# Optimization experiments

Measured on AMD Instinct MI355X. Metric: run time of the kernel, lower is better.

The kernel has to match this reference:

```python
import jax, jax.numpy as jnp
import numpy as np

E = 1024   # embed_dim
H = 16     # num_heads
D = E // H # head_dim = 64
S = 8192   # cache length
LN_EPS = 1e-6  # flax LayerNorm default


def _ln(x, scale, bias):
    m = jnp.mean(x, axis=-1, keepdims=True)
    v = jnp.mean(jnp.square(x - m), axis=-1, keepdims=True)
    return (x - m) * jax.lax.rsqrt(v + LN_EPS) * scale + bias


def setup_inputs() -> dict:
    key = jax.random.key(0)
    ks = jax.random.split(key, 16)
    w = lambda k, shape: jax.random.normal(k, shape, jnp.float32) * 0.02
    return {
        "x": jax.random.normal(ks[0], (E,), jnp.float32),
        "cache": jax.random.normal(ks[1], (2, S, H, D), jnp.float32),
        "Wv": w(ks[2], (E, E)), "bv": jnp.zeros((E,), jnp.float32),
        "Wq": w(ks[3], (E, E)), "bq": jnp.zeros((E,), jnp.float32),
        "Wk": w(ks[4], (E, E)), "bk": jnp.zeros((E,), jnp.float32),
        "Wo": w(ks[5], (E, E)), "bo": jnp.zeros((E,), jnp.float32),
        "W1": w(ks[6], (E, E)), "b1": jnp.zeros((E,), jnp.float32),
        "W2": w(ks[7], (E, E)), "b2": jnp.zeros((E,), jnp.float32),
        "ln1_s": jnp.ones((E,), jnp.float32), "ln1_b": jnp.zeros((E,), jnp.float32),
        "ln2_s": jnp.ones((E,), jnp.float32), "ln2_b": jnp.zeros((E,), jnp.float32),
        "eval_flag": 1,
    }


def reference(x, cache, Wv, bv, Wq, bq, Wk, bk, Wo, bo,
              W1, b1, W2, b2, ln1_s, ln1_b, ln2_s, ln2_b, eval_flag):
    # --- attention with shifting KV cache ---
    v_i = (x @ Wv + bv).reshape(1, H, D)
    q_i = (x @ Wq + bq).reshape(H, D)
    k_i = (x @ Wk + bk).reshape(1, H, D)
    v = jnp.concatenate((cache[0, 1:], v_i), axis=0)  # [S, H, D]
    k = jnp.concatenate((cache[1, 1:], k_i), axis=0)  # [S, H, D]
    mask = jnp.any(v != 0, axis=(1, 2))               # [S]
    attn = jnp.einsum('hd,khd->hk', q_i, k) / jnp.sqrt(jnp.float32(D))
    attn = jnp.where(mask, attn, -jnp.inf)
    attn = jax.nn.softmax(attn, axis=-1)              # [H, S]
    values = jnp.einsum('hk,khd->hd', attn, v).reshape(E)
    out_i = values @ Wo + bo
    new_cache = jnp.stack([v, k])                     # [2, S, H, D]

    # --- residual + LN + FFN (dropout deterministic => identity) ---
    h = _ln(x + out_i, ln1_s, ln1_b)
    ff = jax.nn.relu(h @ W1 + b1) @ W2 + b2
    h = _ln(h + ff, ln2_s, ln2_b)
    return (h, new_cache)
```

## Files before the change

### kernel.cpp

```cpp
#include <hip/hip_runtime.h>
#include <hip/hip_bf16.h>

#define SLEN 8192
#define EDIM 1024
#define NB   1024

typedef float f4 __attribute__((ext_vector_type(4)));


__device__ inline float2 blockSum256_2(float2 v, float2* lds) {
#pragma unroll
    for (int off = 32; off; off >>= 1) {
        v.x += __shfl_xor(v.x, off);
        v.y += __shfl_xor(v.y, off);
    }
    int w = threadIdx.x >> 6, ln = threadIdx.x & 63;
    __syncthreads();
    if (ln == 0) lds[w] = v;
    __syncthreads();
    float2 s;
    s.x = lds[0].x + lds[1].x + lds[2].x + lds[3].x;
    s.y = lds[0].y + lds[1].y + lds[2].y + lds[3].y;
    return s;
}

__device__ inline float2 blockSum1024_2(float2 v, float2* lds) {
#pragma unroll
    for (int off = 32; off; off >>= 1) {
        v.x += __shfl_xor(v.x, off);
        v.y += __shfl_xor(v.y, off);
    }
    int w = threadIdx.x >> 6, ln = threadIdx.x & 63;
    __syncthreads();
    if (ln == 0) lds[w] = v;
    __syncthreads();
    float2 s = {0.f, 0.f};
#pragma unroll
    for (int i = 0; i < 16; ++i) { s.x += lds[i].x; s.y += lds[i].y; }
    return s;
}

__global__ __launch_bounds__(256) void qkv_partial(
    const float* __restrict__ Wq, const float* __restrict__ Wk,
    const float* __restrict__ Wv, const float* __restrict__ x,
    float* __restrict__ part) {
    int cg = blockIdx.x;
    int m = cg >> 2;
    const float* W = (m == 0) ? Wq : ((m == 1) ? Wk : Wv);
    int col = (cg & 3) * 256 + threadIdx.x;
    int r0 = blockIdx.y * 64;
    float acc = 0.f;
#pragma unroll 8
    for (int r = 0; r < 64; ++r)
        acc = fmaf(x[r0 + r], W[(r0 + r) * EDIM + col], acc);
    part[((size_t)m * 16 + blockIdx.y) * EDIM + col] = acc;
}

__global__ __launch_bounds__(1024) void qkv_combine(
    const float* __restrict__ part,
    const float* __restrict__ bq, const float* __restrict__ bk,
    const float* __restrict__ bv,
    float* __restrict__ qs, float* __restrict__ ki, float* __restrict__ vi) {
    int m = blockIdx.x, t = threadIdx.x;
    float v = 0.f;
#pragma unroll
    for (int sl = 0; sl < 16; ++sl) v += part[((size_t)m * 16 + sl) * EDIM + t];
    if (m == 0) qs[t] = (v + bq[t]) * 0.125f;
    else if (m == 1) ki[t] = v + bk[t];
    else vi[t] = v + bv[t];
}

__global__ __launch_bounds__(512) void attn_main(
    const float* __restrict__ cache,
    const float* __restrict__ qs,
    const float* __restrict__ ki, const float* __restrict__ vi,
    float* __restrict__ nv, float* __restrict__ nk,
    float* __restrict__ m2, float* __restrict__ l2, float* __restrict__ acc2) {
    __shared__ float sm[8][16];
    __shared__ float mlM[16], mlL[16];
    __shared__ float sacc[8][16][64];
    int tid = threadIdx.x;
    int w = tid >> 6, ld = tid & 63;
    int s = blockIdx.x * 8 + w;

    bool last = (s >= SLEN - 1);
    const float* vsrc = last ? vi : cache + (size_t)(s + 1) * EDIM;
    const float* ksrc = last ? ki : cache + (size_t)(SLEN + s + 1) * EDIM;

    f4 vv[4], kv[4], q4[4];
#pragma unroll
    for (int it = 0; it < 4; ++it)
        vv[it] = __builtin_nontemporal_load((const f4*)(vsrc + it * 256 + ld * 4));
#pragma unroll
    for (int it = 0; it < 4; ++it)
        kv[it] = __builtin_nontemporal_load((const f4*)(ksrc + it * 256 + ld * 4));
#pragma unroll
    for (int it = 0; it < 4; ++it)
        q4[it] = *(const f4*)(qs + it * 256 + ld * 4);

    unsigned nzb = 0u;
#pragma unroll
    for (int it = 0; it < 4; ++it) {
        __builtin_nontemporal_store(vv[it], (f4*)(nv + (size_t)s * EDIM + it * 256 + ld * 4));
        nzb |= __float_as_uint(vv[it].x) | __float_as_uint(vv[it].y) |
               __float_as_uint(vv[it].z) | __float_as_uint(vv[it].w);
    }
    float sc[4];
#pragma unroll
    for (int it = 0; it < 4; ++it) {
        __builtin_nontemporal_store(kv[it], (f4*)(nk + (size_t)s * EDIM + it * 256 + ld * 4));
        float d = q4[it].x * kv[it].x + q4[it].y * kv[it].y +
                  q4[it].z * kv[it].z + q4[it].w * kv[it].w;
        d += __shfl_xor(d, 1);
        d += __shfl_xor(d, 2);
        d += __shfl_xor(d, 4);
        d += __shfl_xor(d, 8);
        sc[it] = d;
    }
    if (__ballot(nzb != 0u) == 0ull) {
#pragma unroll
        for (int it = 0; it < 4; ++it) sc[it] = -1e30f;
    }
    if ((ld & 15) == 0) {
#pragma unroll
        for (int it = 0; it < 4; ++it) sm[w][it * 4 + (ld >> 4)] = sc[it];
    }
    __syncthreads();

    if (tid < 16) {
        float M = sm[0][tid];
#pragma unroll
        for (int ww = 1; ww < 8; ++ww) M = fmaxf(M, sm[ww][tid]);
        float L = 0.f;
#pragma unroll
        for (int ww = 0; ww < 8; ++ww) L += __expf(sm[ww][tid] - M);
        mlM[tid] = M; mlL[tid] = L;
    }
    __syncthreads();

#pragma unroll
    for (int it = 0; it < 4; ++it) {
        int h = it * 4 + (ld >> 4);
        float wg = __expf(sc[it] - mlM[h]);
        *(f4*)&sacc[w][h][(ld & 15) * 4] =
            (f4){wg * vv[it].x, wg * vv[it].y, wg * vv[it].z, wg * vv[it].w};
    }
    __syncthreads();

#pragma unroll
    for (int j = 0; j < 2; ++j) {
        int h = 2 * w + j;
        float a = 0.f;
#pragma unroll
        for (int ww = 0; ww < 8; ++ww) a += sacc[ww][h][ld];
        acc2[((size_t)blockIdx.x * 16 + h) * 64 + ld] = a;
        if (ld == 0) {
            m2[blockIdx.x * 16 + h] = mlM[h];
            l2[blockIdx.x * 16 + h] = mlL[h];
        }
    }
}

__global__ __launch_bounds__(256) void attn_red(
    const float* __restrict__ m2, const float* __restrict__ l2,
    const float* __restrict__ acc2,
    float* __restrict__ m3, float* __restrict__ l3, float* __restrict__ acc3) {
    __shared__ float sM[4], sL[4], sA[4][64];
    int h = blockIdx.x, g = blockIdx.y;
    int t = threadIdx.x, w = t >> 6, ld = t & 63;
    int p0 = g * 64 + w * 16;

    float mv[16];
#pragma unroll
    for (int i = 0; i < 16; ++i) mv[i] = m2[(p0 + i) * 16 + h];
    float lm = -1e30f;
#pragma unroll
    for (int i = 0; i < 16; ++i) lm = fmaxf(lm, mv[i]);
    float ll = 0.f, la = 0.f;
#pragma unroll
    for (int i = 0; i < 16; ++i) {
        float e = __expf(mv[i] - lm);
        ll += e * l2[(p0 + i) * 16 + h];
        la += e * acc2[(size_t)(p0 + i) * 1024 + (size_t)h * 64 + ld];
    }
    if (ld == 0) { sM[w] = lm; sL[w] = ll; }
    sA[w][ld] = la;
    __syncthreads();
    if (w == 0) {
        float M = fmaxf(fmaxf(sM[0], sM[1]), fmaxf(sM[2], sM[3]));
        float L = 0.f, a = 0.f;
#pragma unroll
        for (int w4 = 0; w4 < 4; ++w4) {
            float e = __expf(sM[w4] - M);
            L += e * sL[w4];
            a += e * sA[w4][ld];
        }
        acc3[((size_t)g * 16 + h) * 64 + ld] = a;
        if (ld == 0) { m3[g * 16 + h] = M; l3[g * 16 + h] = L; }
    }
}

__global__ __launch_bounds__(256) void gemv_wo(
    const float* __restrict__ Wo,
    const float* __restrict__ m3, const float* __restrict__ l3,
    const float* __restrict__ acc3, float* __restrict__ part) {
    __shared__ float vals[64];
    int by = blockIdx.y;
    int t = threadIdx.x;
    float M = -1e30f;
#pragma unroll
    for (int g = 0; g < 16; ++g) M = fmaxf(M, m3[g * 16 + by]);
    float L = 0.f;
#pragma unroll
    for (int g = 0; g < 16; ++g) L += __expf(m3[g * 16 + by] - M) * l3[g * 16 + by];
    if (t < 64) {
        float a = 0.f;
#pragma unroll
        for (int g = 0; g < 16; ++g)
            a += __expf(m3[g * 16 + by] - M) * acc3[((size_t)g * 16 + by) * 64 + t];
        vals[t] = a / L;
    }
    __syncthreads();
    int col = blockIdx.x * 256 + t;
    float acc = 0.f;
#pragma unroll 8
    for (int r = 0; r < 64; ++r)
        acc = fmaf(vals[r], Wo[(size_t)(by * 64 + r) * EDIM + col], acc);
    part[(size_t)by * EDIM + col] = acc;
}

__global__ __launch_bounds__(256) void gemv_w1(
    const float* __restrict__ W1, const float* __restrict__ gp1,
    const float* __restrict__ bo, const float* __restrict__ x,
    const float* __restrict__ ln1s, const float* __restrict__ ln1b,
    float* __restrict__ h1, float* __restrict__ part) {
    __shared__ float r_l[1024];
    __shared__ float2 red[4];
    __shared__ float vals[64];
    int t = threadIdx.x;
    float2 ss = {0.f, 0.f};
#pragma unroll
    for (int j = 0; j < 4; ++j) {
        int i = t + 256 * j;
        float v = x[i] + bo[i];
#pragma unroll
        for (int sl = 0; sl < 16; ++sl) v += gp1[(size_t)sl * EDIM + i];
        r_l[i] = v;
        ss.x += v; ss.y += v * v;
    }
    float2 s = blockSum256_2(ss, red);
    float mean = s.x * (1.f / 1024.f);
    float var = s.y * (1.f / 1024.f) - mean * mean;
    float rstd = rsqrtf(var + 1e-6f);
    int by = blockIdx.y;
    if (t < 64) {
        int row = by * 64 + t;
        float hv = (r_l[row] - mean) * rstd * ln1s[row] + ln1b[row];
        vals[t] = hv;
        if (blockIdx.x == 0) h1[row] = hv;
    }
    __syncthreads();
    int col = blockIdx.x * 256 + t;
    float acc = 0.f;
#pragma unroll 8
    for (int r = 0; r < 64; ++r)
        acc = fmaf(vals[r], W1[(size_t)(by * 64 + r) * EDIM + col], acc);
    part[(size_t)by * EDIM + col] = acc;
}

__global__ __launch_bounds__(256) void gemv_w2(
    const float* __restrict__ W2, const float* __restrict__ gp2,
    const float* __restrict__ b1, float* __restrict__ part) {
    __shared__ float vals[64];
    int by = blockIdx.y;
    int t = threadIdx.x;
    if (t < 64) {
        int r = by * 64 + t;
        float v = b1[r];
#pragma unroll
        for (int sl = 0; sl < 16; ++sl) v += gp2[(size_t)sl * EDIM + r];
        vals[t] = fmaxf(v, 0.f);
    }
    __syncthreads();
    int col = blockIdx.x * 256 + t;
    float acc = 0.f;
#pragma unroll 8
    for (int r = 0; r < 64; ++r)
        acc = fmaf(vals[r], W2[(size_t)(by * 64 + r) * EDIM + col], acc);
    part[(size_t)by * EDIM + col] = acc;
}

__global__ __launch_bounds__(1024) void combine_ln(
    const float* __restrict__ part, const float* __restrict__ bias,
    const float* __restrict__ resid, const float* __restrict__ g,
    const float* __restrict__ b, float* __restrict__ out) {
    __shared__ float2 lds[16];
    int t = threadIdx.x;
    float v = bias[t];
#pragma unroll
    for (int sl = 0; sl < 16; ++sl) v += part[(size_t)sl * EDIM + t];
    float r = resid[t] + v;
    float2 s = blockSum1024_2((float2){r, r * r}, lds);
    float mean = s.x * (1.f / 1024.f);
    float var = s.y * (1.f / 1024.f) - mean * mean;
    out[t] = (r - mean) * rsqrtf(var + 1e-6f) * g[t] + b[t];
}

extern "C" void kernel_launch(void* const* d_in, const int* in_sizes, int n_in,
                              void* d_out, int out_size, void* d_ws, size_t ws_size,
                              hipStream_t stream) {
    const float* x     = (const float*)d_in[0];
    const float* cache = (const float*)d_in[1];
    const float* Wv    = (const float*)d_in[2];
    const float* bv    = (const float*)d_in[3];
    const float* Wq    = (const float*)d_in[4];
    const float* bq    = (const float*)d_in[5];
    const float* Wk    = (const float*)d_in[6];
    const float* bk    = (const float*)d_in[7];
    const float* Wo    = (const float*)d_in[8];
    const float* bo    = (const float*)d_in[9];
    const float* W1    = (const float*)d_in[10];
    const float* b1    = (const float*)d_in[11];
    const float* W2    = (const float*)d_in[12];
    const float* b2    = (const float*)d_in[13];
    const float* ln1s  = (const float*)d_in[14];
    const float* ln1b  = (const float*)d_in[15];
    const float* ln2s  = (const float*)d_in[16];
    const float* ln2b  = (const float*)d_in[17];

    float* out = (float*)d_out;
    float* nv = out + 1024;
    float* nk = out + 1024 + (size_t)SLEN * EDIM;

    float* w      = (float*)d_ws;
    float* qs     = w;
    float* ki     = qs + 1024;
    float* vi     = ki + 1024;
    float* qkvp   = vi + 1024;
    float* m2     = qkvp + 48 * 1024;
    float* l2     = m2 + (size_t)NB * 16;
    float* acc2   = l2 + (size_t)NB * 16;
    float* m3     = acc2 + (size_t)NB * 1024;
    float* l3     = m3 + 256;
    float* acc3   = l3 + 256;
    float* h1     = acc3 + 16 * 1024;
    float* gp1    = h1 + 1024;
    float* gp2    = gp1 + 16 * 1024;
    float* gp3    = gp2 + 16 * 1024;

    qkv_partial<<<dim3(12, 16), 256, 0, stream>>>(Wq, Wk, Wv, x, qkvp);
    qkv_combine<<<3, 1024, 0, stream>>>(qkvp, bq, bk, bv, qs, ki, vi);
    attn_main<<<NB, 512, 0, stream>>>(cache, qs, ki, vi, nv, nk, m2, l2, acc2);
    attn_red<<<dim3(16, 16), 256, 0, stream>>>(m2, l2, acc2, m3, l3, acc3);
    gemv_wo<<<dim3(4, 16), 256, 0, stream>>>(Wo, m3, l3, acc3, gp1);
    gemv_w1<<<dim3(4, 16), 256, 0, stream>>>(W1, gp1, bo, x, ln1s, ln1b, h1, gp2);
    gemv_w2<<<dim3(4, 16), 256, 0, stream>>>(W2, gp2, b1, gp3);
    combine_ln<<<1, 1024, 0, stream>>>(gp3, b2, h1, ln2s, ln2b, out);
}
```

Before: 61.13 us.

## Fold QKV combine into attention and fuse tail kernels into one cooperative launch

The qkv_combine kernel is removed: every attention block now sums the Q partials itself into shared memory, and the last block also builds the new k/v row. The attention reduction, Wo, W1 and W2 GEMVs and the final LayerNorm are merged into one cooperative kernel of 256 blocks separated by grid.sync, cutting eight launches down to three. The aim is to remove launch gaps and inter-kernel drain costs. The cost is redundant Q-partial reads in every attention block and grid-wide barrier overhead.

```diff
diff --git a/kernel.cpp b/kernel.cpp
--- a/kernel.cpp
+++ b/kernel.cpp
@@ -1,5 +1,8 @@
 #include <hip/hip_runtime.h>
+#include <hip/hip_cooperative_groups.h>
 #include <hip/hip_bf16.h>
+
+namespace cg = cooperative_groups;
 
 #define SLEN 8192
 #define EDIM 1024
@@ -24,30 +27,14 @@
     return s;
 }
 
-__device__ inline float2 blockSum1024_2(float2 v, float2* lds) {
-#pragma unroll
-    for (int off = 32; off; off >>= 1) {
-        v.x += __shfl_xor(v.x, off);
-        v.y += __shfl_xor(v.y, off);
-    }
-    int w = threadIdx.x >> 6, ln = threadIdx.x & 63;
-    __syncthreads();
-    if (ln == 0) lds[w] = v;
-    __syncthreads();
-    float2 s = {0.f, 0.f};
-#pragma unroll
-    for (int i = 0; i < 16; ++i) { s.x += lds[i].x; s.y += lds[i].y; }
-    return s;
-}
-
 __global__ __launch_bounds__(256) void qkv_partial(
     const float* __restrict__ Wq, const float* __restrict__ Wk,
     const float* __restrict__ Wv, const float* __restrict__ x,
     float* __restrict__ part) {
-    int cg = blockIdx.x;
-    int m = cg >> 2;
+    int cg_ = blockIdx.x;
+    int m = cg_ >> 2;
     const float* W = (m == 0) ? Wq : ((m == 1) ? Wk : Wv);
-    int col = (cg & 3) * 256 + threadIdx.x;
+    int col = (cg_ & 3) * 256 + threadIdx.x;
     int r0 = blockIdx.y * 64;
     float acc = 0.f;
 #pragma unroll 8
@@ -56,47 +43,68 @@
     part[((size_t)m * 16 + blockIdx.y) * EDIM + col] = acc;
 }
 
-__global__ __launch_bounds__(1024) void qkv_combine(
-    const float* __restrict__ part,
+__global__ __launch_bounds__(512) void attn_main(
+    const float* __restrict__ cache,
+    const float* __restrict__ qkvp,
     const float* __restrict__ bq, const float* __restrict__ bk,
     const float* __restrict__ bv,
-    float* __restrict__ qs, float* __restrict__ ki, float* __restrict__ vi) {
-    int m = blockIdx.x, t = threadIdx.x;
-    float v = 0.f;
-#pragma unroll
-    for (int sl = 0; sl < 16; ++sl) v += part[((size_t)m * 16 + sl) * EDIM + t];
-    if (m == 0) qs[t] = (v + bq[t]) * 0.125f;
-    else if (m == 1) ki[t] = v + bk[t];
-    else vi[t] = v + bv[t];
-}
-
-__global__ __launch_bounds__(512) void attn_main(
-    const float* __restrict__ cache,
-    const float* __restrict__ qs,
-    const float* __restrict__ ki, const float* __restrict__ vi,
     float* __restrict__ nv, float* __restrict__ nk,
     float* __restrict__ m2, float* __restrict__ l2, float* __restrict__ acc2) {
+    __shared__ float qs_l[1024];
     __shared__ float sm[8][16];
     __shared__ float mlM[16], mlL[16];
     __shared__ float sacc[8][16][64];
+    float* kivi = &sacc[0][0][0];
+
     int tid = threadIdx.x;
     int w = tid >> 6, ld = tid & 63;
     int s = blockIdx.x * 8 + w;
 
+#pragma unroll
+    for (int j = 0; j < 2; ++j) {
+        int c = tid + 512 * j;
+        float v = bq[c];
+#pragma unroll
+        for (int sl = 0; sl < 16; ++sl) v += qkvp[sl * EDIM + c];
+        qs_l[c] = v * 0.125f;
+    }
+    if (blockIdx.x == NB - 1) {
+#pragma unroll
+        for (int j = 0; j < 2; ++j) {
+            int c = tid + 512 * j;
+            float vv_ = bv[c], kk_ = bk[c];
+#pragma unroll
+            for (int sl = 0; sl < 16; ++sl) {
+                vv_ += qkvp[(32 + sl) * EDIM + c];
+                kk_ += qkvp[(16 + sl) * EDIM + c];
+            }
+            kivi[c] = vv_;
+            kivi[1024 + c] = kk_;
+        }
+    }
+    __syncthreads();
+
     bool last = (s >= SLEN - 1);
-    const float* vsrc = last ? vi : cache + (size_t)(s + 1) * EDIM;
-    const float* ksrc = last ? ki : cache + (size_t)(SLEN + s + 1) * EDIM;
-
     f4 vv[4], kv[4], q4[4];
+    if (!last) {
+        const float* vsrc = cache + (size_t)(s + 1) * EDIM;
+        const float* ksrc = cache + (size_t)(SLEN + s + 1) * EDIM;
+#pragma unroll
+        for (int it = 0; it < 4; ++it)
+            vv[it] = __builtin_nontemporal_load((const f4*)(vsrc + it * 256 + ld * 4));
+#pragma unroll
+        for (int it = 0; it < 4; ++it)
+            kv[it] = __builtin_nontemporal_load((const f4*)(ksrc + it * 256 + ld * 4));
+    } else {
+#pragma unroll
+        for (int it = 0; it < 4; ++it) {
+            vv[it] = *(const f4*)&kivi[it * 256 + ld * 4];
+            kv[it] = *(const f4*)&kivi[1024 + it * 256 + ld * 4];
+        }
+    }
 #pragma unroll
     for (int it = 0; it < 4; ++it)
-        vv[it] = __builtin_nontemporal_load((const f4*)(vsrc + it * 256 + ld * 4));
-#pragma unroll
-    for (int it = 0; it < 4; ++it)
-        kv[it] = __builtin_nontemporal_load((const f4*)(ksrc + it * 256 + ld * 4));
-#pragma unroll
-    for (int it = 0; it < 4; ++it)
-        q4[it] = *(const f4*)(qs + it * 256 + ld * 4);
+        q4[it] = *(const f4*)&qs_l[it * 256 + ld * 4];
 
     unsigned nzb = 0u;
 #pragma unroll
@@ -161,149 +169,176 @@
     }
 }
 
-__global__ __launch_bounds__(256) void attn_red(
+__global__ __launch_bounds__(256) void tail(
     const float* __restrict__ m2, const float* __restrict__ l2,
     const float* __restrict__ acc2,
-    float* __restrict__ m3, float* __restrict__ l3, float* __restrict__ acc3) {
-    __shared__ float sM[4], sL[4], sA[4][64];
-    int h = blockIdx.x, g = blockIdx.y;
-    int t = threadIdx.x, w = t >> 6, ld = t & 63;
-    int p0 = g * 64 + w * 16;
-
-    float mv[16];
-#pragma unroll
-    for (int i = 0; i < 16; ++i) mv[i] = m2[(p0 + i) * 16 + h];
-    float lm = -1e30f;
-#pragma unroll
-    for (int i = 0; i < 16; ++i) lm = fmaxf(lm, mv[i]);
-    float ll = 0.f, la = 0.f;
-#pragma unroll
-    for (int i = 0; i < 16; ++i) {
-        float e = __expf(mv[i] - lm);
-        ll += e * l2[(p0 + i) * 16 + h];
-        la += e * acc2[(size_t)(p0 + i) * 1024 + (size_t)h * 64 + ld];
-    }
-    if (ld == 0) { sM[w] = lm; sL[w] = ll; }
-    sA[w][ld] = la;
-    __syncthreads();
-    if (w == 0) {
-        float M = fmaxf(fmaxf(sM[0], sM[1]), fmaxf(sM[2], sM[3]));
-        float L = 0.f, a = 0.f;
-#pragma unroll
-        for (int w4 = 0; w4 < 4; ++w4) {
-            float e = __expf(sM[w4] - M);
-            L += e * sL[w4];
-            a += e * sA[w4][ld];
-        }
-        acc3[((size_t)g * 16 + h) * 64 + ld] = a;
-        if (ld == 0) { m3[g * 16 + h] = M; l3[g * 16 + h] = L; }
-    }
-}
-
-__global__ __launch_bounds__(256) void gemv_wo(
-    const float* __restrict__ Wo,
-    const float* __restrict__ m3, const float* __restrict__ l3,
-    const float* __restrict__ acc3, float* __restrict__ part) {
+    const float* __restrict__ Wo, const float* __restrict__ bo,
+    const float* __restrict__ x,
+    const float* __restrict__ ln1s, const float* __restrict__ ln1b,
+    const float* __restrict__ W1, const float* __restrict__ b1,
+    const float* __restrict__ W2, const float* __restrict__ b2,
+    const float* __restrict__ ln2s, const float* __restrict__ ln2b,
+    float* __restrict__ m3, float* __restrict__ l3, float* __restrict__ acc3,
+    float* __restrict__ gp1, float* __restrict__ h1,
+    float* __restrict__ gp2, float* __restrict__ gp3,
+    float* __restrict__ out) {
+    cg::grid_group grid = cg::this_grid();
+    __shared__ float r_l[1024];
+    __shared__ float sred[4][64];
     __shared__ float vals[64];
-    int by = blockIdx.y;
-    int t = threadIdx.x;
-    float M = -1e30f;
-#pragma unroll
-    for (int g = 0; g < 16; ++g) M = fmaxf(M, m3[g * 16 + by]);
-    float L = 0.f;
-#pragma unroll
-    for (int g = 0; g < 16; ++g) L += __expf(m3[g * 16 + by] - M) * l3[g * 16 + by];
-    if (t < 64) {
-        float a = 0.f;
-#pragma unroll
-        for (int g = 0; g < 16; ++g)
-            a += __expf(m3[g * 16 + by] - M) * acc3[((size_t)g * 16 + by) * 64 + t];
-        vals[t] = a / L;
-    }
-    __syncthreads();
-    int col = blockIdx.x * 256 + t;
-    float acc = 0.f;
-#pragma unroll 8
-    for (int r = 0; r < 64; ++r)
-        acc = fmaf(vals[r], Wo[(size_t)(by * 64 + r) * EDIM + col], acc);
-    part[(size_t)by * EDIM + col] = acc;
-}
-
-__global__ __launch_bounds__(256) void gemv_w1(
-    const float* __restrict__ W1, const float* __restrict__ gp1,
-    const float* __restrict__ bo, const float* __restrict__ x,
-    const float* __restrict__ ln1s, const float* __restrict__ ln1b,
-    float* __restrict__ h1, float* __restrict__ part) {
-    __shared__ float r_l[1024];
+    __shared__ float sA[4][64];
+    __shared__ float sM[4], sL[4];
     __shared__ float2 red[4];
-    __shared__ float vals[64];
-    int t = threadIdx.x;
-    float2 ss = {0.f, 0.f};
-#pragma unroll
-    for (int j = 0; j < 4; ++j) {
-        int i = t + 256 * j;
-        float v = x[i] + bo[i];
-#pragma unroll
-        for (int sl = 0; sl < 16; ++sl) v += gp1[(size_t)sl * EDIM + i];
-        r_l[i] = v;
-        ss.x += v; ss.y += v * v;
-    }
-    float2 s = blockSum256_2(ss, red);
-    float mean = s.x * (1.f / 1024.f);
-    float var = s.y * (1.f / 1024.f) - mean * mean;
-    float rstd = rsqrtf(var + 1e-6f);
-    int by = blockIdx.y;
-    if (t < 64) {
-        int row = by * 64 + t;
-        float hv = (r_l[row] - mean) * rstd * ln1s[row] + ln1b[row];
-        vals[t] = hv;
-        if (blockIdx.x == 0) h1[row] = hv;
-    }
-    __syncthreads();
-    int col = blockIdx.x * 256 + t;
-    float acc = 0.f;
-#pragma unroll 8
-    for (int r = 0; r < 64; ++r)
-        acc = fmaf(vals[r], W1[(size_t)(by * 64 + r) * EDIM + col], acc);
-    part[(size_t)by * EDIM + col] = acc;
-}
-
-__global__ __launch_bounds__(256) void gemv_w2(
-    const float* __restrict__ W2, const float* __restrict__ gp2,
-    const float* __restrict__ b1, float* __restrict__ part) {
-    __shared__ float vals[64];
-    int by = blockIdx.y;
-    int t = threadIdx.x;
-    if (t < 64) {
-        int r = by * 64 + t;
-        float v = b1[r];
-#pragma unroll
-        for (int sl = 0; sl < 16; ++sl) v += gp2[(size_t)sl * EDIM + r];
-        vals[t] = fmaxf(v, 0.f);
-    }
-    __syncthreads();
-    int col = blockIdx.x * 256 + t;
-    float acc = 0.f;
-#pragma unroll 8
-    for (int r = 0; r < 64; ++r)
-        acc = fmaf(vals[r], W2[(size_t)(by * 64 + r) * EDIM + col], acc);
-    part[(size_t)by * EDIM + col] = acc;
-}
-
-__global__ __launch_bounds__(1024) void combine_ln(
-    const float* __restrict__ part, const float* __restrict__ bias,
-    const float* __restrict__ resid, const float* __restrict__ g,
-    const float* __restrict__ b, float* __restrict__ out) {
-    __shared__ float2 lds[16];
-    int t = threadIdx.x;
-    float v = bias[t];
-#pragma unroll
-    for (int sl = 0; sl < 16; ++sl) v += part[(size_t)sl * EDIM + t];
-    float r = resid[t] + v;
-    float2 s = blockSum1024_2((float2){r, r * r}, lds);
-    float mean = s.x * (1.f / 1024.f);
-    float var = s.y * (1.f / 1024.f) - mean * mean;
-    out[t] = (r - mean) * rsqrtf(var + 1e-6f) * g[t] + b[t];
+
+    int b = blockIdx.x, t = threadIdx.x, w = t >> 6, ld = t & 63;
+
+    {
+        int h = b >> 4, g = b & 15;
+        int p0 = g * 64 + w * 16;
+        float mv[16];
+#pragma unroll
+        for (int i = 0; i < 16; ++i) mv[i] = m2[(p0 + i) * 16 + h];
+        float lm = -1e30f;
+#pragma unroll
+        for (int i = 0; i < 16; ++i) lm = fmaxf(lm, mv[i]);
+        float ll = 0.f, la = 0.f;
+#pragma unroll
+        for (int i = 0; i < 16; ++i) {
+            float e = __expf(mv[i] - lm);
+            ll += e * l2[(p0 + i) * 16 + h];
+            la += e * acc2[(size_t)(p0 + i) * 1024 + (size_t)h * 64 + ld];
+        }
+        if (ld == 0) { sM[w] = lm; sL[w] = ll; }
+        sA[w][ld] = la;
+        __syncthreads();
+        if (w == 0) {
+            float M = fmaxf(fmaxf(sM[0], sM[1]), fmaxf(sM[2], sM[3]));
+            float L = 0.f, a = 0.f;
+#pragma unroll
+            for (int w4 = 0; w4 < 4; ++w4) {
+                float e = __expf(sM[w4] - M);
+                L += e * sL[w4];
+                a += e * sA[w4][ld];
+            }
+            acc3[((size_t)g * 16 + h) * 64 + ld] = a;
+            if (ld == 0) { m3[g * 16 + h] = M; l3[g * 16 + h] = L; }
+        }
+    }
+    grid.sync();
+
+    {
+        int c = b >> 4, h = b & 15;
+        if (t < 64) {
+            float M = -1e30f;
+#pragma unroll
+            for (int g = 0; g < 16; ++g) M = fmaxf(M, m3[g * 16 + h]);
+            float L = 0.f, a = 0.f;
+#pragma unroll
+            for (int g = 0; g < 16; ++g) {
+                float e = __expf(m3[g * 16 + h] - M);
+                L += e * l3[g * 16 + h];
+                a += e * acc3[((size_t)g * 16 + h) * 64 + t];
+            }
+            vals[t] = a / L;
+        }
+        __syncthreads();
+        int q = t >> 6, j = t & 63;
+        float acc = 0.f;
+#pragma unroll
+        for (int i = 0; i < 16; ++i) {
+            int r = q * 16 + i;
+            acc = fmaf(vals[r], Wo[(size_t)(h * 64 + r) * EDIM + c * 64 + j], acc);
+        }
+        sred[q][j] = acc;
+        __syncthreads();
+        if (t < 64) gp1[h * EDIM + c * 64 + t] =
+            sred[0][t] + sred[1][t] + sred[2][t] + sred[3][t];
+    }
+    grid.sync();
+
+    {
+        int c = b >> 4, r = b & 15;
+        float2 ss = {0.f, 0.f};
+#pragma unroll
+        for (int j = 0; j < 4; ++j) {
+            int i = t + 256 * j;
+            float v = x[i] + bo[i];
+#pragma unroll
+            for (int sl = 0; sl < 16; ++sl) v += gp1[sl * EDIM + i];
+            r_l[i] = v;
+            ss.x += v; ss.y += v * v;
+        }
+        float2 sT = blockSum256_2(ss, red);
+        float mean = sT.x * (1.f / 1024.f);
+        float var = sT.y * (1.f / 1024.f) - mean * mean;
+        float rstd = rsqrtf(var + 1e-6f);
+        if (t < 64) {
+            int row = r * 64 + t;
+            float hv = (r_l[row] - mean) * rstd * ln1s[row] + ln1b[row];
+            vals[t] = hv;
+            if (c == 0) h1[row] = hv;
+        }
+        __syncthreads();
+        int q = t >> 6, j = t & 63;
+        float acc = 0.f;
+#pragma unroll
+        for (int i = 0; i < 16; ++i) {
+            int rr = q * 16 + i;
+            acc = fmaf(vals[rr], W1[(size_t)(r * 64 + rr) * EDIM + c * 64 + j], acc);
+        }
+        sred[q][j] = acc;
+        __syncthreads();
+        if (t < 64) gp2[r * EDIM + c * 64 + t] =
+            sred[0][t] + sred[1][t] + sred[2][t] + sred[3][t];
+    }
+    grid.sync();
+
+    {
+        int c = b >> 4, r = b & 15;
+        if (t < 64) {
+            int row = r * 64 + t;
+            float v = b1[row];
+#pragma unroll
+            for (int sl = 0; sl < 16; ++sl) v += gp2[sl * EDIM + row];
+            vals[t] = fmaxf(v, 0.f);
+        }
+        __syncthreads();
+        int q = t >> 6, j = t & 63;
+        float acc = 0.f;
+#pragma unroll
+        for (int i = 0; i < 16; ++i) {
+            int rr = q * 16 + i;
+            acc = fmaf(vals[rr], W2[(size_t)(r * 64 + rr) * EDIM + c * 64 + j], acc);
+        }
+        sred[q][j] = acc;
+        __syncthreads();
+        if (t < 64) gp3[r * EDIM + c * 64 + t] =
+            sred[0][t] + sred[1][t] + sred[2][t] + sred[3][t];
+    }
+    grid.sync();
+
+    if (b == 0) {
+        float rv[4];
+        float2 ss = {0.f, 0.f};
+#pragma unroll
+        for (int j = 0; j < 4; ++j) {
+            int i = t + 256 * j;
+            float v = b2[i] + h1[i];
+#pragma unroll
+            for (int sl = 0; sl < 16; ++sl) v += gp3[sl * EDIM + i];
+            rv[j] = v;
+            ss.x += v; ss.y += v * v;
+        }
+        float2 sT = blockSum256_2(ss, red);
+        float mean = sT.x * (1.f / 1024.f);
+        float var = sT.y * (1.f / 1024.f) - mean * mean;
+        float rstd = rsqrtf(var + 1e-6f);
+#pragma unroll
+        for (int j = 0; j < 4; ++j) {
+            int i = t + 256 * j;
+            out[i] = (rv[j] - mean) * rstd * ln2s[i] + ln2b[i];
+        }
+    }
 }
 
 extern "C" void kernel_launch(void* const* d_in, const int* in_sizes, int n_in,
@@ -332,28 +367,32 @@
     float* nv = out + 1024;
     float* nk = out + 1024 + (size_t)SLEN * EDIM;
 
-    float* w      = (float*)d_ws;
-    float* qs     = w;
-    float* ki     = qs + 1024;
-    float* vi     = ki + 1024;
-    float* qkvp   = vi + 1024;
-    float* m2     = qkvp + 48 * 1024;
-    float* l2     = m2 + (size_t)NB * 16;
-    float* acc2   = l2 + (size_t)NB * 16;
-    float* m3     = acc2 + (size_t)NB * 1024;
-    float* l3     = m3 + 256;
-    float* acc3   = l3 + 256;
-    float* h1     = acc3 + 16 * 1024;
-    float* gp1    = h1 + 1024;
-    float* gp2    = gp1 + 16 * 1024;
-    float* gp3    = gp2 + 16 * 1024;
+    float* w    = (float*)d_ws;
+    float* qkvp = w;
+    float* m2   = qkvp + 48 * 1024;
+    float* l2   = m2 + (size_t)NB * 16;
+    float* acc2 = l2 + (size_t)NB * 16;
+    float* m3   = acc2 + (size_t)NB * 1024;
+    float* l3   = m3 + 256;
+    float* acc3 = l3 + 256;
+    float* gp1  = acc3 + 16 * 1024;
+    float* h1   = gp1 + 16 * 1024;
+    float* gp2  = h1 + 1024;
+    float* gp3  = gp2 + 16 * 1024;
 
     qkv_partial<<<dim3(12, 16), 256, 0, stream>>>(Wq, Wk, Wv, x, qkvp);
-    qkv_combine<<<3, 1024, 0, stream>>>(qkvp, bq, bk, bv, qs, ki, vi);
-    attn_main<<<NB, 512, 0, stream>>>(cache, qs, ki, vi, nv, nk, m2, l2, acc2);
-    attn_red<<<dim3(16, 16), 256, 0, stream>>>(m2, l2, acc2, m3, l3, acc3);
-    gemv_wo<<<dim3(4, 16), 256, 0, stream>>>(Wo, m3, l3, acc3, gp1);
-    gemv_w1<<<dim3(4, 16), 256, 0, stream>>>(W1, gp1, bo, x, ln1s, ln1b, h1, gp2);
-    gemv_w2<<<dim3(4, 16), 256, 0, stream>>>(W2, gp2, b1, gp3);
-    combine_ln<<<1, 1024, 0, stream>>>(gp3, b2, h1, ln2s, ln2b, out);
-}
+    attn_main<<<NB, 512, 0, stream>>>(cache, qkvp, bq, bk, bv, nv, nk, m2, l2, acc2);
+
+    void* args[] = {
+        (void*)&m2, (void*)&l2, (void*)&acc2,
+        (void*)&Wo, (void*)&bo, (void*)&x,
+        (void*)&ln1s, (void*)&ln1b,
+        (void*)&W1, (void*)&b1, (void*)&W2, (void*)&b2,
+        (void*)&ln2s, (void*)&ln2b,
+        (void*)&m3, (void*)&l3, (void*)&acc3,
+        (void*)&gp1, (void*)&h1, (void*)&gp2, (void*)&gp3,
+        (void*)&out
+    };
+    hipLaunchCooperativeKernel((const void*)tail, dim3(256), dim3(256),
+                               args, 0, stream);
+}
```

Result: slower. 156.9 us (+156.7%).
